# Kernel optimization log

Hardware: AMD Instinct MI355X
Metric: run time of the kernel (lower is better)

Reference implementation:

```python
import jax, jax.numpy as jnp
import numpy as np

L, B, N, D, H = 12, 4, 1024, 768, 12
DH = D // H
HID = 4 * D
R = 2050          # all_num_relative_distance
T = 512           # 1 + max_time_len: time tokens; fft tokens = N - T
SCALE = DH ** -0.5
EPS = 1e-5        # torch LayerNorm default


def _ln(x, w, b):
    m = x.mean(-1, keepdims=True)
    v = ((x - m) ** 2).mean(-1, keepdims=True)
    return (x - m) * jax.lax.rsqrt(v + EPS) * w + b


def setup_inputs():
    key = jax.random.key(0)
    ks = jax.random.split(key, 16)
    g = lambda i, shape, s=0.02: jax.random.normal(ks[i], shape, jnp.float32) * s
    return {
        "x": g(0, (B, N, D), 1.0),
        "mask": jnp.ones((B, N), jnp.bool_),
        "rel_idx": jax.random.randint(ks[1], (N, N), 0, R, jnp.int32),
        "qkv_w": g(2, (L, 3 * D, D)),
        "proj_w": g(3, (L, D, D)),
        "proj_b": jnp.zeros((L, D), jnp.float32),
        "norm1_w": jnp.ones((L, D), jnp.float32),
        "norm1_b": jnp.zeros((L, D), jnp.float32),
        "gamma1": jnp.full((L, D), 0.1, jnp.float32),
        "gamma2": jnp.full((L, D), 0.1, jnp.float32),
        "rel_table": g(4, (L, R, H)),
        "normt_w": jnp.ones((L, D), jnp.float32),
        "normt_b": jnp.zeros((L, D), jnp.float32),
        "fc1t_w": g(5, (L, HID, D)),
        "fc1t_b": jnp.zeros((L, HID), jnp.float32),
        "fc2t_w": g(6, (L, D, HID)),
        "fc2t_b": jnp.zeros((L, D), jnp.float32),
        "normf_w": jnp.ones((L, D), jnp.float32),
        "normf_b": jnp.zeros((L, D), jnp.float32),
        "fc1f_w": g(7, (L, HID, D)),
        "fc1f_b": jnp.zeros((L, HID), jnp.float32),
        "fc2f_w": g(8, (L, D, HID)),
        "fc2f_b": jnp.zeros((L, D), jnp.float32),
    }


def _forward(x, mask, rel_idx, params):
    def mlp(z, nw, nb, w1, b1, w2, b2):
        z = _ln(z, nw, nb)
        z = jax.nn.gelu(z @ w1.T + b1, approximate=False)  # torch nn.GELU (erf)
        return z @ w2.T + b2

    def step(x, p):
        h = _ln(x, p["norm1_w"], p["norm1_b"])
        qkv = (h @ p["qkv_w"].T).reshape(B, N, 3, H, DH).transpose(2, 0, 3, 1, 4)
        q, k, v = qkv[0] * SCALE, qkv[1], qkv[2]
        attn = jnp.einsum("bhqd,bhkd->bhqk", q, k)
        bias = p["rel_table"][rel_idx]                 # [N, N, H]
        attn = attn + jnp.transpose(bias, (2, 0, 1))[None]
        attn = jnp.where(mask[:, None, None, :], attn, -jnp.inf)
        attn = jax.nn.softmax(attn, axis=-1)
        o = jnp.einsum("bhqk,bhkd->bqhd", attn, v).reshape(B, N, D)
        x = x + p["gamma1"] * (o @ p["proj_w"].T + p["proj_b"])
        # dual time/fft MLP branches (mlp_tf is None path)
        xt, xf = x[:, :T], x[:, T:]
        xt = xt + p["gamma2"] * mlp(xt, p["normt_w"], p["normt_b"], p["fc1t_w"], p["fc1t_b"], p["fc2t_w"], p["fc2t_b"])
        xf = xf + p["gamma2"] * mlp(xf, p["normf_w"], p["normf_b"], p["fc1f_w"], p["fc1f_b"], p["fc2f_w"], p["fc2f_b"])
        return jnp.concatenate([xt, xf], axis=1), None

    x, _ = jax.lax.scan(step, x, params)
    return x


def reference(x, mask, rel_idx, qkv_w, proj_w, proj_b, norm1_w, norm1_b, gamma1, gamma2, rel_table, normt_w, normt_b, fc1t_w, fc1t_b, fc2t_w, fc2t_b, normf_w, normf_b, fc1f_w, fc1f_b, fc2f_w, fc2f_b):
    params = dict(qkv_w=qkv_w, proj_w=proj_w, proj_b=proj_b, norm1_w=norm1_w, norm1_b=norm1_b,
                  gamma1=gamma1, gamma2=gamma2, rel_table=rel_table,
                  normt_w=normt_w, normt_b=normt_b, fc1t_w=fc1t_w, fc1t_b=fc1t_b, fc2t_w=fc2t_w, fc2t_b=fc2t_b,
                  normf_w=normf_w, normf_b=normf_b, fc1f_w=fc1f_w, fc1f_b=fc1f_b, fc2f_w=fc2f_w, fc2f_b=fc2f_b)
    return _forward(x, mask, rel_idx, params)
```

## Files before the change

### kernel.cpp

```cpp
#include <hip/hip_runtime.h>
#include <hip/hip_bf16.h>
#include <math.h>

#define NN    1024
#define DDIM  768
#define NHEAD 12
#define DHD   64
#define HIDD  3072
#define RTAB  2050
#define NTOK  4096

using short8 = __attribute__((ext_vector_type(8))) short;
using f32x4  = __attribute__((ext_vector_type(4))) float;
using u16x4  = __attribute__((ext_vector_type(4))) unsigned short;

#define S_QKV   (3*DDIM*DDIM)
#define S_PROJ  (DDIM*DDIM)
#define S_FC    (HIDD*DDIM)
#define W_QKV   0
#define W_PROJ  (S_QKV)
#define W_FC1T  (W_PROJ + S_PROJ)
#define W_FC2T  (W_FC1T + S_FC)
#define W_FC1F  (W_FC2T + S_FC)
#define W_FC2F  (W_FC1F + S_FC)
#define W_TOTAL (W_FC2F + S_FC)

__device__ __forceinline__ void async16(const void* g, void* l) {
  __builtin_amdgcn_global_load_lds(
      (const __attribute__((address_space(1))) void*)g,
      (__attribute__((address_space(3))) void*)l, 16, 0, 0);
}
__device__ __forceinline__ unsigned short bf16bits(float f) {
  __hip_bfloat16 h = __float2bfloat16(f);
  return __builtin_bit_cast(unsigned short, h);
}
__device__ __forceinline__ float bits2f(unsigned short u) {
  __hip_bfloat16 h = __builtin_bit_cast(__hip_bfloat16, u);
  return __bfloat162float(h);
}

__device__ __forceinline__ void stage72(const unsigned short* g, int gstride,
                                        unsigned short* lds, int tid) {
  #pragma unroll
  for (int q = 0; q < 2; q++) {
    int s = q*256 + tid;
    int row = (s*7282) >> 16;
    int c = s - row*9;
    int cc = (c == 8) ? 0 : c;
    async16(g + row*gstride + cc*8, (char*)lds + s*16);
  }
  if (tid < 64) {
    int s = 512 + tid;
    int row = (s*7282) >> 16;
    int c = s - row*9;
    int cc = (c == 8) ? 0 : c;
    async16(g + row*gstride + cc*8, (char*)lds + s*16);
  }
}

__global__ __launch_bounds__(256) void convert6(
    const float* __restrict__ s0, const float* __restrict__ s1,
    const float* __restrict__ s2, const float* __restrict__ s3,
    const float* __restrict__ s4, const float* __restrict__ s5,
    unsigned short* __restrict__ dst)
{
  size_t e = ((size_t)blockIdx.x * 256 + threadIdx.x) * 4;
  if (e >= (size_t)W_TOTAL) return;
  const float* src; size_t off;
  if      (e < (size_t)W_PROJ) { src = s0; off = e; }
  else if (e < (size_t)W_FC1T) { src = s1; off = e - W_PROJ; }
  else if (e < (size_t)W_FC2T) { src = s2; off = e - W_FC1T; }
  else if (e < (size_t)W_FC1F) { src = s3; off = e - W_FC2T; }
  else if (e < (size_t)W_FC2F) { src = s4; off = e - W_FC1F; }
  else                         { src = s5; off = e - W_FC2F; }
  f32x4 f = *(const f32x4*)(src + off);
  u16x4 u;
  u[0] = bf16bits(f[0]); u[1] = bf16bits(f[1]);
  u[2] = bf16bits(f[2]); u[3] = bf16bits(f[3]);
  *(u16x4*)(dst + e) = u;
}

__global__ __launch_bounds__(256) void bias_gather(
    const int* __restrict__ rel_idx, const float* __restrict__ table,
    unsigned short* __restrict__ bias)
{
  int T = blockIdx.x*256 + threadIdx.x;
  int lane = T & 63, wv2 = (T>>6)&3, kt = (T>>8)&15, qt = T>>12;
  int lr = lane & 15, lq = lane >> 4;
  int idx[16];
  #pragma unroll
  for (int j = 0; j < 4; j++)
    #pragma unroll
    for (int r = 0; r < 4; r++) {
      int q = qt*64 + wv2*16 + lq*4 + r;
      int k = kt*64 + j*16 + lr;
      idx[j*4+r] = rel_idx[q*NN + k];
    }
  #pragma unroll
  for (int h = 0; h < NHEAD; h++) {
    unsigned short v16[16];
    #pragma unroll
    for (int e = 0; e < 16; e++)
      v16[e] = bf16bits(table[(size_t)idx[e]*NHEAD + h]);
    size_t off = ((((size_t)h*16 + qt)*16 + kt)*4 + wv2)*1024 + lane*16;
    *(u16x4*)(bias + off)      = *(u16x4*)(v16);
    *(u16x4*)(bias + off + 4)  = *(u16x4*)(v16 + 4);
    *(u16x4*)(bias + off + 8)  = *(u16x4*)(v16 + 8);
    *(u16x4*)(bias + off + 12) = *(u16x4*)(v16 + 12);
  }
}

__global__ __launch_bounds__(256) void ln_kernel(
    const float* __restrict__ X,
    const float* __restrict__ w0, const float* __restrict__ b0,
    const float* __restrict__ w1, const float* __restrict__ b1,
    unsigned short* __restrict__ out, int mode)
{
  int p = blockIdx.x, tid = threadIdx.x;
  int token; const float *wp, *bp;
  if (mode == 0) { token = p; wp = w0; bp = b0; }
  else {
    int hf = p >> 11, rr = p & 2047;
    token = (rr >> 9) * NN + hf * 512 + (rr & 511);
    wp = hf ? w1 : w0; bp = hf ? b1 : b0;
  }
  const float* xr = X + (size_t)token * DDIM;
  float v[3]; float s = 0.f, sq = 0.f;
  #pragma unroll
  for (int k = 0; k < 3; k++) { v[k] = xr[tid + k*256]; s += v[k]; sq += v[k]*v[k]; }
  #pragma unroll
  for (int off = 32; off >= 1; off >>= 1) { s += __shfl_down(s, off); sq += __shfl_down(sq, off); }
  __shared__ float red[8];
  int lane = tid & 63, wid = tid >> 6;
  if (lane == 0) { red[wid] = s; red[4 + wid] = sq; }
  __syncthreads();
  s  = red[0] + red[1] + red[2] + red[3];
  sq = red[4] + red[5] + red[6] + red[7];
  float mean = s * (1.0f/768.0f);
  float var  = sq * (1.0f/768.0f) - mean*mean;
  float rs   = rsqrtf(var + 1e-5f);
  #pragma unroll
  for (int k = 0; k < 3; k++) {
    int idx = tid + k*256;
    out[(size_t)p * DDIM + idx] = bf16bits((v[k]-mean)*rs*wp[idx] + bp[idx]);
  }
}

__global__ __launch_bounds__(256) void gemm_bt(
    const unsigned short* __restrict__ A,
    const unsigned short* __restrict__ B0,
    const unsigned short* __restrict__ B1,
    int M, int N, int K, int mode,
    float* __restrict__ X,
    const float* __restrict__ bias0,
    const float* __restrict__ bias1,
    const float* __restrict__ gamma,
    unsigned short* __restrict__ oq,
    unsigned short* __restrict__ ok,
    unsigned short* __restrict__ ov,
    unsigned short* __restrict__ obf)
{
  __shared__ __align__(16) unsigned short As[128*32];
  __shared__ __align__(16) unsigned short Bs[128*32];
  int tid = threadIdx.x;
  int lane = tid & 63, wv = tid >> 6;
  int wm = wv >> 1, wn = wv & 1;
  int lr = lane & 15, lq = lane >> 4;
  int m0 = blockIdx.y * 128, n0 = blockIdx.x * 128;
  int hf = (m0 >= 2048) ? 1 : 0;
  const unsigned short* Bp = (mode >= 2 && hf) ? B1 : B0;

  f32x4 zero = {0.f, 0.f, 0.f, 0.f};
  f32x4 acc[4][4];
  #pragma unroll
  for (int i = 0; i < 4; i++)
    #pragma unroll
    for (int j = 0; j < 4; j++) acc[i][j] = zero;

  int kper = K / gridDim.z;
  int kbase = blockIdx.z * kper;
  bool addb = (blockIdx.z == 0);
  int nk = kper >> 5;
  for (int kt = 0; kt < nk; kt++) {
    __syncthreads();
    int k0 = kbase + (kt << 5);
    #pragma unroll
    for (int i = 0; i < 2; i++) {
      int bo  = tid*16 + i*4096;
      int row = bo >> 6;
      int col = (bo & 63) >> 1;
      async16(A  + (size_t)(m0+row)*K + k0 + col, (char*)As + bo);
      async16(Bp + (size_t)(n0+row)*K + k0 + col, (char*)Bs + bo);
    }
    __syncthreads();
    short8 af[4], bfv[4];
    #pragma unroll
    for (int i = 0; i < 4; i++) af[i]  = *(const short8*)&As[(wm*64 + i*16 + lr)*32 + lq*8];
    #pragma unroll
    for (int j = 0; j < 4; j++) bfv[j] = *(const short8*)&Bs[(wn*64 + j*16 + lr)*32 + lq*8];
    #pragma unroll
    for (int i = 0; i < 4; i++)
      #pragma unroll
      for (int j = 0; j < 4; j++)
        acc[i][j] = __builtin_amdgcn_mfma_f32_16x16x32_bf16(af[i], bfv[j], acc[i][j], 0, 0, 0);
  }

  #pragma unroll
  for (int j = 0; j < 4; j++) {
    int n = n0 + wn*64 + j*16 + lr;
    if (mode == 0) {
      int which = (n >= 2*DDIM) ? 2 : (n >= DDIM ? 1 : 0);
      int rem = n - which*DDIM;
      int head = rem >> 6, dh = rem & 63;
      float sc = (which == 0) ? 0.125f : 1.0f;
      #pragma unroll
      for (int i = 0; i < 4; i++) {
        int mb = m0 + wm*64 + i*16 + lq*4;
        int b = mb >> 10, t = mb & 1023;
        if (which == 2) {
          u16x4 pk;
          #pragma unroll
          for (int r = 0; r < 4; r++) pk[r] = bf16bits(acc[i][j][r]);
          *(u16x4*)(ov + ((size_t)(b*NHEAD + head)*DHD + dh)*NN + t) = pk;
        } else {
          unsigned short* dst = (which == 0) ? oq : ok;
          #pragma unroll
          for (int r = 0; r < 4; r++)
            dst[(((size_t)b*NHEAD + head)*NN + t + r)*DHD + dh] = bf16bits(acc[i][j][r] * sc);
        }
      }
    } else if (mode == 1) {
      float g = gamma[n];
      float bb = addb ? bias0[n] : 0.f;
      #pragma unroll
      for (int i = 0; i < 4; i++) {
        int mb = m0 + wm*64 + i*16 + lq*4;
        #pragma unroll
        for (int r = 0; r < 4; r++) {
          int m = mb + r;
          atomicAdd(X + (size_t)m*DDIM + n, g*(acc[i][j][r] + bb));
        }
      }
    } else if (mode == 2) {
      const float* bpp = hf ? bias1 : bias0;
      float bb = bpp[n];
      #pragma unroll
      for (int i = 0; i < 4; i++) {
        int mb = m0 + wm*64 + i*16 + lq*4;
        #pragma unroll
        for (int r = 0; r < 4; r++) {
          int m = mb + r;
          float v = acc[i][j][r] + bb;
          float ge = 0.5f * v * (1.0f + erff(v * 0.70710678118f));
          obf[(size_t)m*HIDD + n] = bf16bits(ge);
        }
      }
    } else {
      const float* bpp = hf ? bias1 : bias0;
      float g = gamma[n];
      float bb = addb ? bpp[n] : 0.f;
      #pragma unroll
      for (int i = 0; i < 4; i++) {
        int mb = m0 + wm*64 + i*16 + lq*4;
        #pragma unroll
        for (int r = 0; r < 4; r++) {
          int m = mb + r;
          int rr = m & 2047, b = rr >> 9, tt = rr & 511;
          int token = b*NN + hf*512 + tt;
          atomicAdd(X + (size_t)token*DDIM + n, g*(acc[i][j][r] + bb));
        }
      }
    }
  }
}

__global__ __launch_bounds__(256) void attn_kernel(
    const unsigned short* __restrict__ Q,
    const unsigned short* __restrict__ K,
    const unsigned short* __restrict__ V,
    const unsigned short* __restrict__ BIAS,
    unsigned short* __restrict__ O)
{
  int qt = blockIdx.x, bh = blockIdx.y;
  int h = bh % NHEAD, b = bh / NHEAD;
  int tid = threadIdx.x, lane = tid & 63, wv = tid >> 6;
  int lr = lane & 15, lq = lane >> 4;

  __shared__ __align__(16) unsigned short Qs[64*72];
  __shared__ __align__(16) unsigned short Ks[64*72];
  __shared__ __align__(16) unsigned short Vt[64*72];
  __shared__ __align__(16) unsigned short Ps[4][16*72];

  stage72(Q + ((size_t)bh*NN + qt*64)*DHD, DHD, Qs, tid);
  __syncthreads();
  short8 qf0 = *(const short8*)&Qs[(wv*16 + lr)*72 + lq*8];
  short8 qf1 = *(const short8*)&Qs[(wv*16 + lr)*72 + 32 + lq*8];

  f32x4 zero = {0.f, 0.f, 0.f, 0.f};
  f32x4 Oacc[4];
  #pragma unroll
  for (int jj = 0; jj < 4; jj++) Oacc[jj] = zero;
  float lsum[4] = {0.f, 0.f, 0.f, 0.f};

  const unsigned short* Kb = K + (size_t)bh*NN*DHD;
  const unsigned short* Vb = V + (size_t)bh*DHD*NN;
  const unsigned short* biasL = BIAS + (((size_t)h*16 + qt)*16)*4096 + wv*1024 + lane*16;

  for (int kt = 0; kt < 16; kt++) {
    __syncthreads();
    stage72(Kb + (size_t)kt*64*DHD, DHD, Ks, tid);
    stage72(Vb + kt*64, NN, Vt, tid);
    const unsigned short* bp = biasL + kt*4096;
    short8 bb0 = *(const short8*)bp;
    short8 bb1 = *(const short8*)(bp + 8);
    __syncthreads();

    f32x4 S[4];
    #pragma unroll
    for (int j = 0; j < 4; j++) S[j] = zero;
    #pragma unroll
    for (int j = 0; j < 4; j++) {
      short8 kf0 = *(const short8*)&Ks[(j*16 + lr)*72 + lq*8];
      short8 kf1 = *(const short8*)&Ks[(j*16 + lr)*72 + 32 + lq*8];
      S[j] = __builtin_amdgcn_mfma_f32_16x16x32_bf16(qf0, kf0, S[j], 0, 0, 0);
      S[j] = __builtin_amdgcn_mfma_f32_16x16x32_bf16(qf1, kf1, S[j], 0, 0, 0);
    }
    #pragma unroll
    for (int j = 0; j < 4; j++) {
      #pragma unroll
      for (int r = 0; r < 4; r++) {
        int e = j*4 + r;
        unsigned short bu = (unsigned short)((e < 8) ? bb0[e] : bb1[e-8]);
        float p = __expf(S[j][r] + bits2f(bu));
        S[j][r] = p;
        lsum[r] += p;
      }
    }
    #pragma unroll
    for (int j = 0; j < 4; j++)
      #pragma unroll
      for (int r = 0; r < 4; r++)
        Ps[wv][(lq*4 + r)*72 + j*16 + lr] = bf16bits(S[j][r]);

    short8 pf0 = *(const short8*)&Ps[wv][lr*72 + lq*8];
    short8 pf1 = *(const short8*)&Ps[wv][lr*72 + 32 + lq*8];
    #pragma unroll
    for (int jj = 0; jj < 4; jj++) {
      short8 vf0 = *(const short8*)&Vt[(jj*16 + lr)*72 + lq*8];
      short8 vf1 = *(const short8*)&Vt[(jj*16 + lr)*72 + 32 + lq*8];
      Oacc[jj] = __builtin_amdgcn_mfma_f32_16x16x32_bf16(pf0, vf0, Oacc[jj], 0, 0, 0);
      Oacc[jj] = __builtin_amdgcn_mfma_f32_16x16x32_bf16(pf1, vf1, Oacc[jj], 0, 0, 0);
    }
  }
  #pragma unroll
  for (int r = 0; r < 4; r++) {
    float l = lsum[r];
    l += __shfl_xor(l, 1); l += __shfl_xor(l, 2);
    l += __shfl_xor(l, 4); l += __shfl_xor(l, 8);
    lsum[r] = 1.0f / l;
  }
  #pragma unroll
  for (int jj = 0; jj < 4; jj++)
    #pragma unroll
    for (int r = 0; r < 4; r++) {
      int q = qt*64 + wv*16 + lq*4 + r;
      int token = b*NN + q;
      O[(size_t)token*DDIM + h*DHD + jj*16 + lr] = bf16bits(Oacc[jj][r] * lsum[r]);
    }
}

extern "C" void kernel_launch(void* const* d_in, const int* in_sizes, int n_in,
                              void* d_out, int out_size, void* d_ws, size_t ws_size,
                              hipStream_t stream)
{
  const float* x_in      = (const float*)d_in[0];
  const int*   rel_idx   = (const int*)d_in[2];
  const float* qkv_w     = (const float*)d_in[3];
  const float* proj_w    = (const float*)d_in[4];
  const float* proj_b    = (const float*)d_in[5];
  const float* norm1_w   = (const float*)d_in[6];
  const float* norm1_b   = (const float*)d_in[7];
  const float* gamma1    = (const float*)d_in[8];
  const float* gamma2    = (const float*)d_in[9];
  const float* rel_table = (const float*)d_in[10];
  const float* normt_w   = (const float*)d_in[11];
  const float* normt_b   = (const float*)d_in[12];
  const float* fc1t_w    = (const float*)d_in[13];
  const float* fc1t_b    = (const float*)d_in[14];
  const float* fc2t_w    = (const float*)d_in[15];
  const float* fc2t_b    = (const float*)d_in[16];
  const float* normf_w   = (const float*)d_in[17];
  const float* normf_b   = (const float*)d_in[18];
  const float* fc1f_w    = (const float*)d_in[19];
  const float* fc1f_b    = (const float*)d_in[20];
  const float* fc2f_w    = (const float*)d_in[21];
  const float* fc2f_b    = (const float*)d_in[22];

  float* X = (float*)d_out;

  unsigned short* wbf     = (unsigned short*)d_ws;
  unsigned short* h_bf    = wbf  + W_TOTAL;
  unsigned short* q_bf    = h_bf + (size_t)NTOK*DDIM;
  unsigned short* k_bf    = q_bf + (size_t)NTOK*DDIM;
  unsigned short* v_bf    = k_bf + (size_t)NTOK*DDIM;
  unsigned short* o_bf    = v_bf + (size_t)NTOK*DDIM;
  unsigned short* bias_bf = o_bf + (size_t)NTOK*DDIM;
  unsigned short* g1_bf   = bias_bf;

  hipMemcpyAsync(X, x_in, (size_t)NTOK*DDIM*sizeof(float),
                 hipMemcpyDeviceToDevice, stream);

  for (int l = 0; l < 12; l++) {
    convert6<<<11520, 256, 0, stream>>>(
        qkv_w  + (size_t)l*S_QKV,  proj_w + (size_t)l*S_PROJ,
        fc1t_w + (size_t)l*S_FC,   fc2t_w + (size_t)l*S_FC,
        fc1f_w + (size_t)l*S_FC,   fc2f_w + (size_t)l*S_FC, wbf);

    bias_gather<<<256, 256, 0, stream>>>(
        rel_idx, rel_table + (size_t)l*RTAB*NHEAD, bias_bf);

    ln_kernel<<<4096, 256, 0, stream>>>(
        X, norm1_w + l*DDIM, norm1_b + l*DDIM, nullptr, nullptr, h_bf, 0);

    gemm_bt<<<dim3(18, 32), 256, 0, stream>>>(
        h_bf, wbf + W_QKV, nullptr, NTOK, 3*DDIM, DDIM, 0,
        nullptr, nullptr, nullptr, nullptr, q_bf, k_bf, v_bf, nullptr);

    attn_kernel<<<dim3(16, 48), 256, 0, stream>>>(q_bf, k_bf, v_bf, bias_bf, o_bf);

    gemm_bt<<<dim3(6, 32, 2), 256, 0, stream>>>(
        o_bf, wbf + W_PROJ, nullptr, NTOK, DDIM, DDIM, 1,
        X, proj_b + l*DDIM, nullptr, gamma1 + l*DDIM,
        nullptr, nullptr, nullptr, nullptr);

    ln_kernel<<<4096, 256, 0, stream>>>(
        X, normt_w + l*DDIM, normt_b + l*DDIM,
        normf_w + l*DDIM, normf_b + l*DDIM, h_bf, 1);

    gemm_bt<<<dim3(24, 32), 256, 0, stream>>>(
        h_bf, wbf + W_FC1T, wbf + W_FC1F, NTOK, HIDD, DDIM, 2,
        nullptr, fc1t_b + (size_t)l*HIDD, fc1f_b + (size_t)l*HIDD, nullptr,
        nullptr, nullptr, nullptr, g1_bf);

    gemm_bt<<<dim3(6, 32, 2), 256, 0, stream>>>(
        g1_bf, wbf + W_FC2T, wbf + W_FC2F, NTOK, DDIM, HIDD, 3,
        X, fc2t_b + l*DDIM, fc2f_b + l*DDIM, gamma2 + l*DDIM,
        nullptr, nullptr, nullptr, nullptr);
  }
}
```

Before: 3.136 ms.

## Pipeline GEMM with triple-buffered async LDS loads, swizzle, and 256-row tiles

```diff
diff --git a/kernel.cpp b/kernel.cpp
--- a/kernel.cpp
+++ b/kernel.cpp
@@ -24,6 +24,11 @@
 #define W_FC1F  (W_FC2T + S_FC)
 #define W_FC2F  (W_FC1F + S_FC)
 #define W_TOTAL (W_FC2F + S_FC)
+
+#define SBAR()   asm volatile("s_barrier" ::: "memory")
+#define VMCNT3() asm volatile("s_waitcnt vmcnt(3)" ::: "memory")
+#define VMCNT0() asm volatile("s_waitcnt vmcnt(0)" ::: "memory")
+#define LGKM0()  asm volatile("s_waitcnt lgkmcnt(0)" ::: "memory")
 
 __device__ __forceinline__ void async16(const void* g, void* l) {
   __builtin_amdgcn_global_load_lds(
@@ -146,7 +151,7 @@
   }
 }
 
-__global__ __launch_bounds__(256) void gemm_bt(
+__global__ __launch_bounds__(512, 2) void gemm_bt2(
     const unsigned short* __restrict__ A,
     const unsigned short* __restrict__ B0,
     const unsigned short* __restrict__ B1,
@@ -160,16 +165,39 @@
     unsigned short* __restrict__ ov,
     unsigned short* __restrict__ obf)
 {
-  __shared__ __align__(16) unsigned short As[128*32];
-  __shared__ __align__(16) unsigned short Bs[128*32];
+  __shared__ __align__(16) unsigned short As[3][256*32];
+  __shared__ __align__(16) unsigned short Bs[3][128*32];
+
   int tid = threadIdx.x;
   int lane = tid & 63, wv = tid >> 6;
   int wm = wv >> 1, wn = wv & 1;
   int lr = lane & 15, lq = lane >> 4;
-  int m0 = blockIdx.y * 128, n0 = blockIdx.x * 128;
+  int m0 = blockIdx.y * 256, n0 = blockIdx.x * 128;
   int hf = (m0 >= 2048) ? 1 : 0;
   const unsigned short* Bp = (mode >= 2 && hf) ? B1 : B0;
 
+  int bs0 = tid * 16;
+  int sl0 = bs0 ^ (((bs0 >> 7) & 3) << 4);
+  int bs1 = bs0 + 8192;
+  int sl1 = bs1 ^ (((bs1 >> 7) & 3) << 4);
+  int ar0 = sl0 >> 6, ac0 = (sl0 & 63) >> 1;
+  int ar1 = sl1 >> 6, ac1 = (sl1 & 63) >> 1;
+  const unsigned short* pA0 = A  + (size_t)(m0 + ar0) * K + ac0;
+  const unsigned short* pA1 = A  + (size_t)(m0 + ar1) * K + ac1;
+  const unsigned short* pB  = Bp + (size_t)(n0 + ar0) * K + ac0;
+
+  int offA[4], offB[4];
+  #pragma unroll
+  for (int i = 0; i < 4; i++) {
+    int ra = wm*64 + i*16 + lr;
+    offA[i] = (ra*64 + lq*16) ^ (((ra >> 1) & 3) << 4);
+  }
+  #pragma unroll
+  for (int j = 0; j < 4; j++) {
+    int rb = wn*64 + j*16 + lr;
+    offB[j] = (rb*64 + lq*16) ^ (((rb >> 1) & 3) << 4);
+  }
+
   f32x4 zero = {0.f, 0.f, 0.f, 0.f};
   f32x4 acc[4][4];
   #pragma unroll
@@ -177,32 +205,58 @@
     #pragma unroll
     for (int j = 0; j < 4; j++) acc[i][j] = zero;
 
-  int kper = K / gridDim.z;
+  int kper  = K / gridDim.z;
   int kbase = blockIdx.z * kper;
   bool addb = (blockIdx.z == 0);
   int nk = kper >> 5;
-  for (int kt = 0; kt < nk; kt++) {
-    __syncthreads();
-    int k0 = kbase + (kt << 5);
-    #pragma unroll
-    for (int i = 0; i < 2; i++) {
-      int bo  = tid*16 + i*4096;
-      int row = bo >> 6;
-      int col = (bo & 63) >> 1;
-      async16(A  + (size_t)(m0+row)*K + k0 + col, (char*)As + bo);
-      async16(Bp + (size_t)(n0+row)*K + k0 + col, (char*)Bs + bo);
-    }
-    __syncthreads();
+
+  {
+    int k0 = kbase;
+    async16(pA0 + k0, (char*)&As[0][0] + bs0);
+    async16(pA1 + k0, (char*)&As[0][0] + bs1);
+    async16(pB  + k0, (char*)&Bs[0][0] + bs0);
+    k0 += 32;
+    async16(pA0 + k0, (char*)&As[1][0] + bs0);
+    async16(pA1 + k0, (char*)&As[1][0] + bs1);
+    async16(pB  + k0, (char*)&Bs[1][0] + bs0);
+  }
+  VMCNT3();
+  SBAR();
+
+  int cur = 0;
+  for (int t = 0; t < nk; ++t) {
+    const char* Ab = (const char*)&As[cur][0];
+    const char* Bb = (const char*)&Bs[cur][0];
     short8 af[4], bfv[4];
     #pragma unroll
-    for (int i = 0; i < 4; i++) af[i]  = *(const short8*)&As[(wm*64 + i*16 + lr)*32 + lq*8];
-    #pragma unroll
-    for (int j = 0; j < 4; j++) bfv[j] = *(const short8*)&Bs[(wn*64 + j*16 + lr)*32 + lq*8];
+    for (int i = 0; i < 4; i++) af[i]  = *(const short8*)(Ab + offA[i]);
+    #pragma unroll
+    for (int j = 0; j < 4; j++) bfv[j] = *(const short8*)(Bb + offB[j]);
+
+    if (t + 2 < nk) {
+      int nxt = cur + 2; if (nxt >= 3) nxt -= 3;
+      int k0 = kbase + (t + 2) * 32;
+      async16(pA0 + k0, (char*)&As[nxt][0] + bs0);
+      async16(pA1 + k0, (char*)&As[nxt][0] + bs1);
+      async16(pB  + k0, (char*)&Bs[nxt][0] + bs0);
+      VMCNT3();
+    } else {
+      VMCNT0();
+    }
+    SBAR();
+    LGKM0();
+    __builtin_amdgcn_sched_barrier(0);
+
+    __builtin_amdgcn_s_setprio(1);
     #pragma unroll
     for (int i = 0; i < 4; i++)
       #pragma unroll
       for (int j = 0; j < 4; j++)
         acc[i][j] = __builtin_amdgcn_mfma_f32_16x16x32_bf16(af[i], bfv[j], acc[i][j], 0, 0, 0);
+    __builtin_amdgcn_s_setprio(0);
+    SBAR();
+
+    cur = cur + 1; if (cur >= 3) cur = 0;
   }
 
   #pragma unroll
@@ -216,17 +270,17 @@
       #pragma unroll
       for (int i = 0; i < 4; i++) {
         int mb = m0 + wm*64 + i*16 + lq*4;
-        int b = mb >> 10, t = mb & 1023;
+        int b = mb >> 10, tk = mb & 1023;
         if (which == 2) {
           u16x4 pk;
           #pragma unroll
           for (int r = 0; r < 4; r++) pk[r] = bf16bits(acc[i][j][r]);
-          *(u16x4*)(ov + ((size_t)(b*NHEAD + head)*DHD + dh)*NN + t) = pk;
+          *(u16x4*)(ov + ((size_t)(b*NHEAD + head)*DHD + dh)*NN + tk) = pk;
         } else {
           unsigned short* dst = (which == 0) ? oq : ok;
           #pragma unroll
           for (int r = 0; r < 4; r++)
-            dst[(((size_t)b*NHEAD + head)*NN + t + r)*DHD + dh] = bf16bits(acc[i][j][r] * sc);
+            dst[(((size_t)b*NHEAD + head)*NN + tk + r)*DHD + dh] = bf16bits(acc[i][j][r] * sc);
         }
       }
     } else if (mode == 1) {
@@ -422,13 +476,13 @@
     ln_kernel<<<4096, 256, 0, stream>>>(
         X, norm1_w + l*DDIM, norm1_b + l*DDIM, nullptr, nullptr, h_bf, 0);
 
-    gemm_bt<<<dim3(18, 32), 256, 0, stream>>>(
+    gemm_bt2<<<dim3(18, 16), 512, 0, stream>>>(
         h_bf, wbf + W_QKV, nullptr, NTOK, 3*DDIM, DDIM, 0,
         nullptr, nullptr, nullptr, nullptr, q_bf, k_bf, v_bf, nullptr);
 
     attn_kernel<<<dim3(16, 48), 256, 0, stream>>>(q_bf, k_bf, v_bf, bias_bf, o_bf);
 
-    gemm_bt<<<dim3(6, 32, 2), 256, 0, stream>>>(
+    gemm_bt2<<<dim3(6, 16, 2), 512, 0, stream>>>(
         o_bf, wbf + W_PROJ, nullptr, NTOK, DDIM, DDIM, 1,
         X, proj_b + l*DDIM, nullptr, gamma1 + l*DDIM,
         nullptr, nullptr, nullptr, nullptr);
@@ -437,12 +491,12 @@
         X, normt_w + l*DDIM, normt_b + l*DDIM,
         normf_w + l*DDIM, normf_b + l*DDIM, h_bf, 1);
 
-    gemm_bt<<<dim3(24, 32), 256, 0, stream>>>(
+    gemm_bt2<<<dim3(24, 16), 512, 0, stream>>>(
         h_bf, wbf + W_FC1T, wbf + W_FC1F, NTOK, HIDD, DDIM, 2,
         nullptr, fc1t_b + (size_t)l*HIDD, fc1f_b + (size_t)l*HIDD, nullptr,
         nullptr, nullptr, nullptr, g1_bf);
 
-    gemm_bt<<<dim3(6, 32, 2), 256, 0, stream>>>(
+    gemm_bt2<<<dim3(6, 16, 2), 512, 0, stream>>>(
         g1_bf, wbf + W_FC2T, wbf + W_FC2F, NTOK, DDIM, HIDD, 3,
         X, fc2t_b + l*DDIM, fc2f_b + l*DDIM, gamma2 + l*DDIM,
         nullptr, nullptr, nullptr, nullptr);
```

Measured after the change: 3.069 ms. 2.1% less time.
